# Kernel tuning notes

Measured on AMD Instinct MI355X. Metric: run time of the kernel, lower is better.

## Reference

```python
import jax, jax.numpy as jnp
import numpy as np

N_NODES = 100000
N_EDGES = 1600000
IN_F, HID, OUT_F, K = 64, 64, 16, 3


def gcn_conv(x, src, dst, deg_inv_sqrt, W, b):
    """One PyG-style GCNConv with precomputed self-loop-augmented edges & norm.
    x: [N, Fin]; src/dst: [E+N]; W: [Fin, Fout]; b: [Fout]."""
    h = x @ W                                  # [N, Fout]
    norm = deg_inv_sqrt[src] * deg_inv_sqrt[dst]  # [E+N]
    msg = h[src] * norm[:, None]               # gather + scale  [E+N, Fout]
    out = jax.ops.segment_sum(msg, dst, num_segments=x.shape[0])  # scatter-add
    return out + b


def _prep_edges(edge_index, n):
    loop = jnp.arange(n, dtype=edge_index.dtype)
    src = jnp.concatenate([edge_index[0], loop])
    dst = jnp.concatenate([edge_index[1], loop])
    deg = jax.ops.segment_sum(jnp.ones_like(dst, dtype=jnp.float32), dst, num_segments=n)
    deg_inv_sqrt = jnp.where(deg > 0, jax.lax.rsqrt(jnp.maximum(deg, 1.0)), 0.0)
    return src, dst, deg_inv_sqrt


def setup_inputs() -> dict:
    key = jax.random.key(0)
    ks = jax.random.split(key, 10)
    x = jax.random.normal(ks[0], (N_NODES, IN_F), dtype=jnp.float32)
    edge_index = jax.random.randint(ks[1], (2, N_EDGES), 0, N_NODES, dtype=jnp.int32)
    # Glorot-ish init for weights, zeros for biases (PyG default)
    def glorot(k, fin, fout):
        s = float(np.sqrt(6.0 / (fin + fout)))
        return jax.random.uniform(k, (fin, fout), jnp.float32, -s, s)
    W_in = glorot(ks[2], IN_F, HID)
    b_in = jnp.zeros((HID,), jnp.float32)
    W_h = jnp.stack([glorot(ks[3 + i], HID, HID) for i in range(K - 1)])  # [K-1, HID, HID]
    b_h = jnp.zeros((K - 1, HID), jnp.float32)
    W_out = glorot(ks[3 + K], HID, OUT_F)
    b_out = jnp.zeros((OUT_F,), jnp.float32)
    return {"x": x, "edge_index": edge_index, "W_in": W_in, "b_in": b_in,
            "W_h": W_h, "b_h": b_h, "W_out": W_out, "b_out": b_out}


def reference(x, edge_index, W_in, b_in, W_h, b_h, W_out, b_out):
    src, dst, dis = _prep_edges(edge_index, x.shape[0])
    h = jax.nn.relu(gcn_conv(x, src, dst, dis, W_in, b_in))
    for i in range(W_h.shape[0]):
        h = jax.nn.relu(gcn_conv(h, src, dst, dis, W_h[i], b_h[i]))
    return gcn_conv(h, src, dst, dis, W_out, b_out)
```

## Files before the change

### kernel.cpp

```cpp
#include <hip/hip_runtime.h>


#define BKT_SHIFT 7
#define BKT_NODES 128
#define NBMAX 800
#define EPT 16

typedef __attribute__((ext_vector_type(8))) short short8;
typedef __attribute__((ext_vector_type(4))) float f32x4;

union U4S8 { uint4 u; short8 s; };
__device__ __forceinline__ short8 as_s8(uint4 u) { U4S8 c; c.u = u; return c.s; }

__device__ __forceinline__ unsigned bf16rne(float f) {
    unsigned u = __float_as_uint(f);
    return (u + 0x7FFFu + ((u >> 16) & 1u)) >> 16;
}
__device__ __forceinline__ unsigned pack2(float a, float b) {
    return bf16rne(a) | (bf16rne(b) << 16);
}
__device__ __forceinline__ float lo16(unsigned u) { return __uint_as_float(u << 16); }
__device__ __forceinline__ float hi16(unsigned u) { return __uint_as_float(u & 0xFFFF0000u); }

__global__ __launch_bounds__(256) void k_bcount(const int* __restrict__ dst, int e,
                                                int* __restrict__ bcnt, int nb) {
    __shared__ int l[NBMAX];
    int tdx = threadIdx.x;
    for (int i = tdx; i < nb; i += 256) l[i] = 0;
    __syncthreads();
    int base = blockIdx.x * (256 * EPT);
#pragma unroll
    for (int k = 0; k < EPT; ++k) {
        int i = base + k * 256 + tdx;
        if (i < e) atomicAdd(&l[dst[i] >> BKT_SHIFT], 1);
    }
    __syncthreads();
    for (int i = tdx; i < nb; i += 256) {
        int c = l[i];
        if (c) atomicAdd(&bcnt[i], c);
    }
}

__global__ void k_bscan(const int* __restrict__ bcnt, int* __restrict__ bkt_off,
                        int* __restrict__ gcursor, int nb, int e) {
    __shared__ int lds[256];
    int tdx = threadIdx.x;
    int v[4], s = 0;
#pragma unroll
    for (int k = 0; k < 4; ++k) { int idx = tdx * 4 + k; v[k] = (idx < nb) ? bcnt[idx] : 0; s += v[k]; }
    lds[tdx] = s;
    __syncthreads();
    for (int off = 1; off < 256; off <<= 1) {
        int x = (tdx >= off) ? lds[tdx - off] : 0;
        __syncthreads();
        if (tdx >= off) lds[tdx] += x;
        __syncthreads();
    }
    int run = lds[tdx] - s;
#pragma unroll
    for (int k = 0; k < 4; ++k) {
        int idx = tdx * 4 + k;
        if (idx < nb) { bkt_off[idx] = run; gcursor[idx] = run; }
        run += v[k];
    }
    if (tdx == 0) bkt_off[nb] = e;
}

__global__ __launch_bounds__(256) void k_binB(const int* __restrict__ src,
                                              const int* __restrict__ dst, int e, int nb,
                                              int* __restrict__ gcursor,
                                              unsigned* __restrict__ bkt_edges) {
    __shared__ int lcnt[NBMAX];
    __shared__ int lbase[NBMAX];
    int tdx = threadIdx.x;
    for (int i = tdx; i < nb; i += 256) lcnt[i] = 0;
    __syncthreads();
    int base = blockIdx.x * (256 * EPT);
    unsigned val[EPT];
    int bkt[EPT];
#pragma unroll
    for (int k = 0; k < EPT; ++k) {
        int i = base + k * 256 + tdx;
        if (i < e) {
            int s_ = src[i], d_ = dst[i];
            val[k] = ((unsigned)s_ << BKT_SHIFT) | (unsigned)(d_ & (BKT_NODES - 1));
            bkt[k] = d_ >> BKT_SHIFT;
            atomicAdd(&lcnt[bkt[k]], 1);
        } else bkt[k] = -1;
    }
    __syncthreads();
    for (int b = tdx; b < nb; b += 256) {
        int c = lcnt[b];
        lbase[b] = c ? atomicAdd(&gcursor[b], c) : 0;
        lcnt[b] = 0;
    }
    __syncthreads();
#pragma unroll
    for (int k = 0; k < EPT; ++k) {
        if (bkt[k] >= 0) {
            int o = atomicAdd(&lcnt[bkt[k]], 1);
            bkt_edges[lbase[bkt[k]] + o] = val[k];
        }
    }
}

__global__ __launch_bounds__(256) void k_bsort(
    const int* __restrict__ bkt_off, const unsigned* __restrict__ bkt_edges,
    int* __restrict__ row_ptr, int* __restrict__ csr_src, float* __restrict__ dis,
    int n, int e, int nb) {
    __shared__ int hist[BKT_NODES];
    __shared__ int sc[BKT_NODES];
    __shared__ int cur[BKT_NODES];
    int b = blockIdx.x, tdx = threadIdx.x;
    int beg = bkt_off[b], end = bkt_off[b + 1];
    if (tdx < BKT_NODES) hist[tdx] = 0;
    __syncthreads();
    for (int j = beg + tdx; j < end; j += 256)
        atomicAdd(&hist[bkt_edges[j] & (BKT_NODES - 1)], 1);
    __syncthreads();
    if (tdx < BKT_NODES) sc[tdx] = hist[tdx];
    __syncthreads();
    for (int off = 1; off < BKT_NODES; off <<= 1) {
        int v = (tdx < BKT_NODES && tdx >= off) ? sc[tdx - off] : 0;
        __syncthreads();
        if (tdx < BKT_NODES && tdx >= off) sc[tdx] += v;
        __syncthreads();
    }
    if (tdx < BKT_NODES) {
        int node = b * BKT_NODES + tdx;
        if (node < n) {
            int pos = beg + sc[tdx] - hist[tdx];
            row_ptr[node] = pos;
            cur[tdx] = pos;
            dis[node] = rsqrtf((float)(hist[tdx] + 1));
        }
    }
    if (b == nb - 1 && tdx == 0) row_ptr[n] = e;
    __syncthreads();
    for (int j = beg + tdx; j < end; j += 256) {
        unsigned ev = bkt_edges[j];
        int p = atomicAdd(&cur[ev & (BKT_NODES - 1)], 1);
        csr_src[p] = (int)(ev >> BKT_SHIFT);
    }
}

__global__ void k_cvtX(const float4* __restrict__ x, uint2* __restrict__ hb, int n16) {
    int i = blockIdx.x * 256 + threadIdx.x;
    if (i < n16) {
        float4 v = x[i];
        hb[i] = make_uint2(pack2(v.x, v.y), pack2(v.z, v.w));
    }
}

__global__ void k_cvtW(const float* __restrict__ W, unsigned short* __restrict__ Wt) {
    int i = blockIdx.x * 256 + threadIdx.x;
    int col = i >> 6, k = i & 63;
    Wt[i] = (unsigned short)bf16rne(W[(size_t)k * 64 + col]);
}

__global__ __launch_bounds__(256) void k_mmfma(
    const uint4* __restrict__ hb,
    const uint4* __restrict__ Wt,
    const float* __restrict__ dis,
    unsigned short* __restrict__ t,
    int n) {
    int wave = threadIdx.x >> 6;
    int lane = threadIdx.x & 63;
    int base = blockIdx.x * 64 + wave * 16;
    if (base >= n) return;
    int l15 = lane & 15, lq = lane >> 4;

    int arow = base + l15;
    int arowc = arow < n ? arow : n - 1;
    short8 a0 = as_s8(hb[(size_t)arowc * 8 + lq]);
    short8 a1 = as_s8(hb[(size_t)arowc * 8 + 4 + lq]);

    int orow0 = base + lq * 4;
    float dn[4];
#pragma unroll
    for (int r = 0; r < 4; ++r) {
        int rr = orow0 + r;
        dn[r] = (rr < n) ? dis[rr] : 0.f;
    }

#pragma unroll
    for (int c = 0; c < 4; ++c) {
        short8 b0 = as_s8(Wt[(size_t)(c * 16 + l15) * 8 + lq]);
        short8 b1 = as_s8(Wt[(size_t)(c * 16 + l15) * 8 + 4 + lq]);
        f32x4 acc = {0.f, 0.f, 0.f, 0.f};
        acc = __builtin_amdgcn_mfma_f32_16x16x32_bf16(a0, b0, acc, 0, 0, 0);
        acc = __builtin_amdgcn_mfma_f32_16x16x32_bf16(a1, b1, acc, 0, 0, 0);
#pragma unroll
        for (int r = 0; r < 4; ++r) {
            int row = orow0 + r;
            if (row < n)
                t[(size_t)row * 64 + c * 16 + l15] = (unsigned short)bf16rne(acc[r] * dn[r]);
        }
    }
}

__global__ __launch_bounds__(256) void k_matmul16(
    const uint4* __restrict__ hb, const float* __restrict__ W,
    const float* __restrict__ dis, unsigned* __restrict__ tb, int n) {
    int row = blockIdx.x * 256 + threadIdx.x;
    if (row >= n) return;
    const float4* __restrict__ W4 = (const float4*)W;
    float4 acc[4];
#pragma unroll
    for (int j = 0; j < 4; ++j) acc[j] = make_float4(0.f, 0.f, 0.f, 0.f);
    for (int kq = 0; kq < 8; ++kq) {
        uint4 hv = hb[(size_t)row * 8 + kq];
        float xs[8];
        xs[0] = lo16(hv.x); xs[1] = hi16(hv.x); xs[2] = lo16(hv.y); xs[3] = hi16(hv.y);
        xs[4] = lo16(hv.z); xs[5] = hi16(hv.z); xs[6] = lo16(hv.w); xs[7] = hi16(hv.w);
#pragma unroll
        for (int j = 0; j < 8; ++j) {
            const float4* wr = W4 + (size_t)(kq * 8 + j) * 4;
            float4 w0 = wr[0], w1 = wr[1], w2 = wr[2], w3 = wr[3];
            acc[0].x = fmaf(xs[j], w0.x, acc[0].x); acc[0].y = fmaf(xs[j], w0.y, acc[0].y);
            acc[0].z = fmaf(xs[j], w0.z, acc[0].z); acc[0].w = fmaf(xs[j], w0.w, acc[0].w);
            acc[1].x = fmaf(xs[j], w1.x, acc[1].x); acc[1].y = fmaf(xs[j], w1.y, acc[1].y);
            acc[1].z = fmaf(xs[j], w1.z, acc[1].z); acc[1].w = fmaf(xs[j], w1.w, acc[1].w);
            acc[2].x = fmaf(xs[j], w2.x, acc[2].x); acc[2].y = fmaf(xs[j], w2.y, acc[2].y);
            acc[2].z = fmaf(xs[j], w2.z, acc[2].z); acc[2].w = fmaf(xs[j], w2.w, acc[2].w);
            acc[3].x = fmaf(xs[j], w3.x, acc[3].x); acc[3].y = fmaf(xs[j], w3.y, acc[3].y);
            acc[3].z = fmaf(xs[j], w3.z, acc[3].z); acc[3].w = fmaf(xs[j], w3.w, acc[3].w);
        }
    }
    float dn = dis[row];
    uint4* __restrict__ tr = (uint4*)(tb + (size_t)row * 8);
    uint4 o0;
    o0.x = pack2(acc[0].x * dn, acc[0].y * dn);
    o0.y = pack2(acc[0].z * dn, acc[0].w * dn);
    o0.z = pack2(acc[1].x * dn, acc[1].y * dn);
    o0.w = pack2(acc[1].z * dn, acc[1].w * dn);
    uint4 o1;
    o1.x = pack2(acc[2].x * dn, acc[2].y * dn);
    o1.y = pack2(acc[2].z * dn, acc[2].w * dn);
    o1.z = pack2(acc[3].x * dn, acc[3].y * dn);
    o1.w = pack2(acc[3].z * dn, acc[3].w * dn);
    tr[0] = o0;
    tr[1] = o1;
}

__global__ void k_gather64(const int* __restrict__ row_ptr, const int* __restrict__ csr_src,
                           const uint2* __restrict__ t2, const float* __restrict__ dis,
                           const float* __restrict__ b, uint2* __restrict__ hb2, int n) {
    int tid  = blockIdx.x * blockDim.x + threadIdx.x;
    int node = tid >> 4;
    if (node >= n) return;
    int lane15  = threadIdx.x & 15;
    int grpbase = threadIdx.x & 48;
    int beg = row_ptr[node], end = row_ptr[node + 1];

    uint2 sv0 = t2[(size_t)node * 16 + lane15];
    float4 acc = make_float4(lo16(sv0.x), hi16(sv0.x), lo16(sv0.y), hi16(sv0.y));

    for (int j0 = beg; j0 < end; j0 += 16) {
        int myj = j0 + lane15;
        int sv  = (myj < end) ? csr_src[myj] : 0;
        int m   = end - j0; if (m > 16) m = 16;
        int k = 0;
        for (; k + 4 <= m; k += 4) {
            int s0 = __shfl(sv, grpbase + k);
            int s1 = __shfl(sv, grpbase + k + 1);
            int s2 = __shfl(sv, grpbase + k + 2);
            int s3 = __shfl(sv, grpbase + k + 3);
            uint2 v0 = t2[(size_t)s0 * 16 + lane15];
            uint2 v1 = t2[(size_t)s1 * 16 + lane15];
            uint2 v2 = t2[(size_t)s2 * 16 + lane15];
            uint2 v3 = t2[(size_t)s3 * 16 + lane15];
            acc.x += lo16(v0.x); acc.y += hi16(v0.x); acc.z += lo16(v0.y); acc.w += hi16(v0.y);
            acc.x += lo16(v1.x); acc.y += hi16(v1.x); acc.z += lo16(v1.y); acc.w += hi16(v1.y);
            acc.x += lo16(v2.x); acc.y += hi16(v2.x); acc.z += lo16(v2.y); acc.w += hi16(v2.y);
            acc.x += lo16(v3.x); acc.y += hi16(v3.x); acc.z += lo16(v3.y); acc.w += hi16(v3.y);
        }
        for (; k < m; ++k) {
            int s0 = __shfl(sv, grpbase + k);
            uint2 v0 = t2[(size_t)s0 * 16 + lane15];
            acc.x += lo16(v0.x); acc.y += hi16(v0.x); acc.z += lo16(v0.y); acc.w += hi16(v0.y);
        }
    }
    float dn = dis[node];
    const float4 bb = *(const float4*)(b + lane15 * 4);
    float ox = fmaxf(fmaf(dn, acc.x, bb.x), 0.f);
    float oy = fmaxf(fmaf(dn, acc.y, bb.y), 0.f);
    float oz = fmaxf(fmaf(dn, acc.z, bb.z), 0.f);
    float ow = fmaxf(fmaf(dn, acc.w, bb.w), 0.f);
    hb2[(size_t)node * 16 + lane15] = make_uint2(pack2(ox, oy), pack2(oz, ow));
}

__global__ void k_gather16(const int* __restrict__ row_ptr, const int* __restrict__ csr_src,
                           const uint2* __restrict__ t2, const float* __restrict__ dis,
                           const float* __restrict__ b, float* __restrict__ out, int n) {
    int tid  = blockIdx.x * blockDim.x + threadIdx.x;
    int node = tid >> 2;
    if (node >= n) return;
    int lane3   = threadIdx.x & 3;
    int grpbase = threadIdx.x & 60;
    int beg = row_ptr[node], end = row_ptr[node + 1];

    uint2 sv0 = t2[(size_t)node * 4 + lane3];
    float4 acc = make_float4(lo16(sv0.x), hi16(sv0.x), lo16(sv0.y), hi16(sv0.y));

    for (int j0 = beg; j0 < end; j0 += 4) {
        int myj = j0 + lane3;
        int sv  = (myj < end) ? csr_src[myj] : 0;
        int m   = end - j0; if (m > 4) m = 4;
        int k = 0;
        for (; k + 2 <= m; k += 2) {
            int s0 = __shfl(sv, grpbase + k);
            int s1 = __shfl(sv, grpbase + k + 1);
            uint2 v0 = t2[(size_t)s0 * 4 + lane3];
            uint2 v1 = t2[(size_t)s1 * 4 + lane3];
            acc.x += lo16(v0.x); acc.y += hi16(v0.x); acc.z += lo16(v0.y); acc.w += hi16(v0.y);
            acc.x += lo16(v1.x); acc.y += hi16(v1.x); acc.z += lo16(v1.y); acc.w += hi16(v1.y);
        }
        for (; k < m; ++k) {
            int s0 = __shfl(sv, grpbase + k);
            uint2 v0 = t2[(size_t)s0 * 4 + lane3];
            acc.x += lo16(v0.x); acc.y += hi16(v0.x); acc.z += lo16(v0.y); acc.w += hi16(v0.y);
        }
    }
    float dn = dis[node];
    const float4 bb = *(const float4*)(b + lane3 * 4);
    float4 o;
    o.x = fmaf(dn, acc.x, bb.x);
    o.y = fmaf(dn, acc.y, bb.y);
    o.z = fmaf(dn, acc.z, bb.z);
    o.w = fmaf(dn, acc.w, bb.w);
    *(float4*)(out + (size_t)node * 16 + lane3 * 4) = o;
}


extern "C" void kernel_launch(void* const* d_in, const int* in_sizes, int n_in,
                              void* d_out, int out_size, void* d_ws, size_t ws_size,
                              hipStream_t stream) {
    const float* x     = (const float*)d_in[0];
    const int*   ei    = (const int*)d_in[1];
    const float* W_in  = (const float*)d_in[2];
    const float* b_in  = (const float*)d_in[3];
    const float* W_h   = (const float*)d_in[4];
    const float* b_h   = (const float*)d_in[5];
    const float* W_out = (const float*)d_in[6];
    const float* b_out = (const float*)d_in[7];

    const int n = in_sizes[0] / 64;
    const int e = in_sizes[1] / 2;
    const int* src = ei;
    const int* dst = ei + e;
    const int nb = (n + BKT_NODES - 1) / BKT_NODES;
    if (nb > NBMAX) return;

    char* ws = (char*)d_ws;
    size_t off = 0;
    auto alloc = [&](size_t bytes) { void* p = ws + off; off += (bytes + 255) & ~(size_t)255; return p; };
    float*          dis       = (float*)alloc((size_t)n * 4);
    unsigned short* hb        = (unsigned short*)alloc((size_t)n * 64 * 2);
    unsigned short* t         = (unsigned short*)alloc((size_t)n * 64 * 2);
    unsigned short* Wt        = (unsigned short*)alloc(3 * 4096 * 2);
    int*            bcnt      = (int*)alloc((size_t)nb * 4);
    int*            bkt_off   = (int*)alloc(((size_t)nb + 1) * 4);
    int*            gcursor   = (int*)alloc((size_t)nb * 4);
    unsigned*       bkt_edges = (unsigned*)alloc((size_t)e * 4);
    int*            row_ptr   = (int*)alloc(((size_t)n + 1) * 4);
    int*            csr_src   = (int*)alloc((size_t)e * 4);

    const int nblk_e = (e + 256 * EPT - 1) / (256 * EPT);
    const int nblk_m = (n + 63) / 64;

    hipMemsetAsync(bcnt, 0, (size_t)nb * 4, stream);
    k_bcount<<<nblk_e, 256, 0, stream>>>(dst, e, bcnt, nb);
    k_bscan <<<1, 256, 0, stream>>>(bcnt, bkt_off, gcursor, nb, e);
    k_binB  <<<nblk_e, 256, 0, stream>>>(src, dst, e, nb, gcursor, bkt_edges);
    k_bsort <<<nb, 256, 0, stream>>>(bkt_off, bkt_edges, row_ptr, csr_src, dis, n, e, nb);

    k_cvtW<<<16, 256, 0, stream>>>(W_in, Wt);
    k_cvtW<<<16, 256, 0, stream>>>(W_h, Wt + 4096);
    k_cvtW<<<16, 256, 0, stream>>>(W_h + 4096, Wt + 2 * 4096);
    k_cvtX<<<(n * 16 + 255) / 256, 256, 0, stream>>>((const float4*)x, (uint2*)hb, n * 16);

    k_mmfma<<<nblk_m, 256, 0, stream>>>((const uint4*)hb, (const uint4*)Wt, dis, t, n);
    k_gather64<<<(n * 16 + 255) / 256, 256, 0, stream>>>(row_ptr, csr_src, (const uint2*)t,
                                                         dis, b_in, (uint2*)hb, n);

    for (int l = 0; l < 2; ++l) {
        k_mmfma<<<nblk_m, 256, 0, stream>>>((const uint4*)hb, (const uint4*)(Wt + (1 + l) * 4096),
                                            dis, t, n);
        k_gather64<<<(n * 16 + 255) / 256, 256, 0, stream>>>(row_ptr, csr_src, (const uint2*)t,
                                                             dis, b_h + (size_t)l * 64,
                                                             (uint2*)hb, n);
    }

    k_matmul16<<<(n + 255) / 256, 256, 0, stream>>>((const uint4*)hb, W_out, dis, (unsigned*)t, n);
    k_gather16<<<(n * 4 + 255) / 256, 256, 0, stream>>>(row_ptr, csr_src, (const uint2*)t,
                                                        dis, b_out, (float*)d_out, n);
}
```

Baseline: 249.6 us.

## Fuse gather aggregation with next layer's MFMA matmul via LDS tile

After: 208.6 us. 16.4% less time.

```diff
diff --git a/kernel.cpp b/kernel.cpp
--- a/kernel.cpp
+++ b/kernel.cpp
@@ -144,36 +144,42 @@
     }
 }
 
-__global__ void k_cvtX(const float4* __restrict__ x, uint2* __restrict__ hb, int n16) {
+__global__ void k_cvtW(const float* __restrict__ W_in, const float* __restrict__ W_h,
+                       const float* __restrict__ W_out, unsigned short* __restrict__ Wt) {
     int i = blockIdx.x * 256 + threadIdx.x;
-    if (i < n16) {
-        float4 v = x[i];
-        hb[i] = make_uint2(pack2(v.x, v.y), pack2(v.z, v.w));
-    }
-}
-
-__global__ void k_cvtW(const float* __restrict__ W, unsigned short* __restrict__ Wt) {
-    int i = blockIdx.x * 256 + threadIdx.x;
-    int col = i >> 6, k = i & 63;
-    Wt[i] = (unsigned short)bf16rne(W[(size_t)k * 64 + col]);
-}
-
-__global__ __launch_bounds__(256) void k_mmfma(
-    const uint4* __restrict__ hb,
+    if (i < 12288) {
+        int w = i >> 12, r = i & 4095;
+        int col = r >> 6, k = r & 63;
+        const float* Wp = (w == 0) ? W_in : W_h + (size_t)(w - 1) * 4096;
+        Wt[i] = (unsigned short)bf16rne(Wp[(size_t)k * 64 + col]);
+    } else if (i < 13312) {
+        int r = i - 12288;
+        int col = r >> 6, k = r & 63;
+        Wt[i] = (unsigned short)bf16rne(W_out[(size_t)k * 16 + col]);
+    }
+}
+
+__global__ __launch_bounds__(256) void k_mmfma_x(
+    const float4* __restrict__ x4,
     const uint4* __restrict__ Wt,
     const float* __restrict__ dis,
-    unsigned short* __restrict__ t,
-    int n) {
-    int wave = threadIdx.x >> 6;
-    int lane = threadIdx.x & 63;
+    unsigned short* __restrict__ t, int n) {
+    int wave = threadIdx.x >> 6, lane = threadIdx.x & 63;
     int base = blockIdx.x * 64 + wave * 16;
     if (base >= n) return;
     int l15 = lane & 15, lq = lane >> 4;
 
     int arow = base + l15;
-    int arowc = arow < n ? arow : n - 1;
-    short8 a0 = as_s8(hb[(size_t)arowc * 8 + lq]);
-    short8 a1 = as_s8(hb[(size_t)arowc * 8 + 4 + lq]);
+    int ac = arow < n ? arow : n - 1;
+    const float4* xr = x4 + (size_t)ac * 16;
+    float4 f0 = xr[lq * 2], f1 = xr[lq * 2 + 1];
+    float4 f2 = xr[8 + lq * 2], f3 = xr[9 + lq * 2];
+    uint4 u0, u1;
+    u0.x = pack2(f0.x, f0.y); u0.y = pack2(f0.z, f0.w);
+    u0.z = pack2(f1.x, f1.y); u0.w = pack2(f1.z, f1.w);
+    u1.x = pack2(f2.x, f2.y); u1.y = pack2(f2.z, f2.w);
+    u1.z = pack2(f3.x, f3.y); u1.w = pack2(f3.z, f3.w);
+    short8 a0 = as_s8(u0), a1 = as_s8(u1);
 
     int orow0 = base + lq * 4;
     float dn[4];
@@ -182,7 +188,6 @@
         int rr = orow0 + r;
         dn[r] = (rr < n) ? dis[rr] : 0.f;
     }
-
 #pragma unroll
     for (int c = 0; c < 4; ++c) {
         short8 b0 = as_s8(Wt[(size_t)(c * 16 + l15) * 8 + lq]);
@@ -199,95 +204,95 @@
     }
 }
 
-__global__ __launch_bounds__(256) void k_matmul16(
-    const uint4* __restrict__ hb, const float* __restrict__ W,
-    const float* __restrict__ dis, unsigned* __restrict__ tb, int n) {
-    int row = blockIdx.x * 256 + threadIdx.x;
-    if (row >= n) return;
-    const float4* __restrict__ W4 = (const float4*)W;
-    float4 acc[4];
-#pragma unroll
-    for (int j = 0; j < 4; ++j) acc[j] = make_float4(0.f, 0.f, 0.f, 0.f);
-    for (int kq = 0; kq < 8; ++kq) {
-        uint4 hv = hb[(size_t)row * 8 + kq];
-        float xs[8];
-        xs[0] = lo16(hv.x); xs[1] = hi16(hv.x); xs[2] = lo16(hv.y); xs[3] = hi16(hv.y);
-        xs[4] = lo16(hv.z); xs[5] = hi16(hv.z); xs[6] = lo16(hv.w); xs[7] = hi16(hv.w);
-#pragma unroll
-        for (int j = 0; j < 8; ++j) {
-            const float4* wr = W4 + (size_t)(kq * 8 + j) * 4;
-            float4 w0 = wr[0], w1 = wr[1], w2 = wr[2], w3 = wr[3];
-            acc[0].x = fmaf(xs[j], w0.x, acc[0].x); acc[0].y = fmaf(xs[j], w0.y, acc[0].y);
-            acc[0].z = fmaf(xs[j], w0.z, acc[0].z); acc[0].w = fmaf(xs[j], w0.w, acc[0].w);
-            acc[1].x = fmaf(xs[j], w1.x, acc[1].x); acc[1].y = fmaf(xs[j], w1.y, acc[1].y);
-            acc[1].z = fmaf(xs[j], w1.z, acc[1].z); acc[1].w = fmaf(xs[j], w1.w, acc[1].w);
-            acc[2].x = fmaf(xs[j], w2.x, acc[2].x); acc[2].y = fmaf(xs[j], w2.y, acc[2].y);
-            acc[2].z = fmaf(xs[j], w2.z, acc[2].z); acc[2].w = fmaf(xs[j], w2.w, acc[2].w);
-            acc[3].x = fmaf(xs[j], w3.x, acc[3].x); acc[3].y = fmaf(xs[j], w3.y, acc[3].y);
-            acc[3].z = fmaf(xs[j], w3.z, acc[3].z); acc[3].w = fmaf(xs[j], w3.w, acc[3].w);
-        }
-    }
-    float dn = dis[row];
-    uint4* __restrict__ tr = (uint4*)(tb + (size_t)row * 8);
-    uint4 o0;
-    o0.x = pack2(acc[0].x * dn, acc[0].y * dn);
-    o0.y = pack2(acc[0].z * dn, acc[0].w * dn);
-    o0.z = pack2(acc[1].x * dn, acc[1].y * dn);
-    o0.w = pack2(acc[1].z * dn, acc[1].w * dn);
-    uint4 o1;
-    o1.x = pack2(acc[2].x * dn, acc[2].y * dn);
-    o1.y = pack2(acc[2].z * dn, acc[2].w * dn);
-    o1.z = pack2(acc[3].x * dn, acc[3].y * dn);
-    o1.w = pack2(acc[3].z * dn, acc[3].w * dn);
-    tr[0] = o0;
-    tr[1] = o1;
-}
-
-__global__ void k_gather64(const int* __restrict__ row_ptr, const int* __restrict__ csr_src,
-                           const uint2* __restrict__ t2, const float* __restrict__ dis,
-                           const float* __restrict__ b, uint2* __restrict__ hb2, int n) {
-    int tid  = blockIdx.x * blockDim.x + threadIdx.x;
-    int node = tid >> 4;
-    if (node >= n) return;
-    int lane15  = threadIdx.x & 15;
-    int grpbase = threadIdx.x & 48;
-    int beg = row_ptr[node], end = row_ptr[node + 1];
-
-    uint2 sv0 = t2[(size_t)node * 16 + lane15];
-    float4 acc = make_float4(lo16(sv0.x), hi16(sv0.x), lo16(sv0.y), hi16(sv0.y));
-
-    for (int j0 = beg; j0 < end; j0 += 16) {
-        int myj = j0 + lane15;
-        int sv  = (myj < end) ? csr_src[myj] : 0;
-        int m   = end - j0; if (m > 16) m = 16;
-        int k = 0;
-        for (; k + 4 <= m; k += 4) {
-            int s0 = __shfl(sv, grpbase + k);
-            int s1 = __shfl(sv, grpbase + k + 1);
-            int s2 = __shfl(sv, grpbase + k + 2);
-            int s3 = __shfl(sv, grpbase + k + 3);
-            uint2 v0 = t2[(size_t)s0 * 16 + lane15];
-            uint2 v1 = t2[(size_t)s1 * 16 + lane15];
-            uint2 v2 = t2[(size_t)s2 * 16 + lane15];
-            uint2 v3 = t2[(size_t)s3 * 16 + lane15];
-            acc.x += lo16(v0.x); acc.y += hi16(v0.x); acc.z += lo16(v0.y); acc.w += hi16(v0.y);
-            acc.x += lo16(v1.x); acc.y += hi16(v1.x); acc.z += lo16(v1.y); acc.w += hi16(v1.y);
-            acc.x += lo16(v2.x); acc.y += hi16(v2.x); acc.z += lo16(v2.y); acc.w += hi16(v2.y);
-            acc.x += lo16(v3.x); acc.y += hi16(v3.x); acc.z += lo16(v3.y); acc.w += hi16(v3.y);
-        }
-        for (; k < m; ++k) {
-            int s0 = __shfl(sv, grpbase + k);
-            uint2 v0 = t2[(size_t)s0 * 16 + lane15];
-            acc.x += lo16(v0.x); acc.y += hi16(v0.x); acc.z += lo16(v0.y); acc.w += hi16(v0.y);
-        }
-    }
-    float dn = dis[node];
-    const float4 bb = *(const float4*)(b + lane15 * 4);
-    float ox = fmaxf(fmaf(dn, acc.x, bb.x), 0.f);
-    float oy = fmaxf(fmaf(dn, acc.y, bb.y), 0.f);
-    float oz = fmaxf(fmaf(dn, acc.z, bb.z), 0.f);
-    float ow = fmaxf(fmaf(dn, acc.w, bb.w), 0.f);
-    hb2[(size_t)node * 16 + lane15] = make_uint2(pack2(ox, oy), pack2(oz, ow));
+template<int NC>
+__global__ __launch_bounds__(256) void k_fused(
+    const int* __restrict__ row_ptr, const int* __restrict__ csr_src,
+    const uint2* __restrict__ t_in,
+    const float* __restrict__ dis, const float* __restrict__ bias,
+    const uint4* __restrict__ Wt,
+    unsigned short* __restrict__ t_out, int n) {
+    __shared__ unsigned short htile[64][72];
+
+    int tdx = threadIdx.x;
+    int grp = tdx >> 4, l15 = tdx & 15;
+    int grpbase = tdx & 48;
+    int nblk0 = blockIdx.x * 64;
+
+    const float4 bb = *(const float4*)(bias + l15 * 4);
+
+#pragma unroll
+    for (int rnd = 0; rnd < 4; ++rnd) {
+        int nl = rnd * 16 + grp;
+        int node = nblk0 + nl;
+        uint2 hw = make_uint2(0u, 0u);
+        if (node < n) {
+            int beg = row_ptr[node], end = row_ptr[node + 1];
+            uint2 sv0 = t_in[(size_t)node * 16 + l15];
+            float4 acc = make_float4(lo16(sv0.x), hi16(sv0.x), lo16(sv0.y), hi16(sv0.y));
+            for (int j0 = beg; j0 < end; j0 += 16) {
+                int myj = j0 + l15;
+                int sv  = (myj < end) ? csr_src[myj] : 0;
+                int m   = end - j0; if (m > 16) m = 16;
+                int k = 0;
+                for (; k + 4 <= m; k += 4) {
+                    int s0 = __shfl(sv, grpbase + k);
+                    int s1 = __shfl(sv, grpbase + k + 1);
+                    int s2 = __shfl(sv, grpbase + k + 2);
+                    int s3 = __shfl(sv, grpbase + k + 3);
+                    uint2 v0 = t_in[(size_t)s0 * 16 + l15];
+                    uint2 v1 = t_in[(size_t)s1 * 16 + l15];
+                    uint2 v2 = t_in[(size_t)s2 * 16 + l15];
+                    uint2 v3 = t_in[(size_t)s3 * 16 + l15];
+                    acc.x += lo16(v0.x); acc.y += hi16(v0.x); acc.z += lo16(v0.y); acc.w += hi16(v0.y);
+                    acc.x += lo16(v1.x); acc.y += hi16(v1.x); acc.z += lo16(v1.y); acc.w += hi16(v1.y);
+                    acc.x += lo16(v2.x); acc.y += hi16(v2.x); acc.z += lo16(v2.y); acc.w += hi16(v2.y);
+                    acc.x += lo16(v3.x); acc.y += hi16(v3.x); acc.z += lo16(v3.y); acc.w += hi16(v3.y);
+                }
+                for (; k < m; ++k) {
+                    int s0 = __shfl(sv, grpbase + k);
+                    uint2 v0 = t_in[(size_t)s0 * 16 + l15];
+                    acc.x += lo16(v0.x); acc.y += hi16(v0.x); acc.z += lo16(v0.y); acc.w += hi16(v0.y);
+                }
+            }
+            float dn = dis[node];
+            float ox = fmaxf(fmaf(dn, acc.x, bb.x), 0.f);
+            float oy = fmaxf(fmaf(dn, acc.y, bb.y), 0.f);
+            float oz = fmaxf(fmaf(dn, acc.z, bb.z), 0.f);
+            float ow = fmaxf(fmaf(dn, acc.w, bb.w), 0.f);
+            hw = make_uint2(pack2(ox, oy), pack2(oz, ow));
+        }
+        *(uint2*)&htile[nl][l15 * 4] = hw;
+    }
+    __syncthreads();
+
+    int wave = tdx >> 6, lane = tdx & 63;
+    int lq = lane >> 4;
+    int rbase = wave * 16;
+    short8 a0 = as_s8(*(const uint4*)&htile[rbase + l15][lq * 8]);
+    short8 a1 = as_s8(*(const uint4*)&htile[rbase + l15][32 + lq * 8]);
+
+    int orow0 = nblk0 + rbase + lq * 4;
+    float dn[4];
+#pragma unroll
+    for (int r = 0; r < 4; ++r) {
+        int rr = orow0 + r;
+        dn[r] = (rr < n) ? dis[rr] : 0.f;
+    }
+#pragma unroll
+    for (int c = 0; c < NC; ++c) {
+        short8 b0 = as_s8(Wt[(size_t)(c * 16 + l15) * 8 + lq]);
+        short8 b1 = as_s8(Wt[(size_t)(c * 16 + l15) * 8 + 4 + lq]);
+        f32x4 acc = {0.f, 0.f, 0.f, 0.f};
+        acc = __builtin_amdgcn_mfma_f32_16x16x32_bf16(a0, b0, acc, 0, 0, 0);
+        acc = __builtin_amdgcn_mfma_f32_16x16x32_bf16(a1, b1, acc, 0, 0, 0);
+#pragma unroll
+        for (int r = 0; r < 4; ++r) {
+            int row = orow0 + r;
+            if (row < n)
+                t_out[(size_t)row * (NC * 16) + c * 16 + l15] =
+                    (unsigned short)bf16rne(acc[r] * dn[r]);
+        }
+    }
 }
 
 __global__ void k_gather16(const int* __restrict__ row_ptr, const int* __restrict__ csr_src,
@@ -356,9 +361,9 @@
     size_t off = 0;
     auto alloc = [&](size_t bytes) { void* p = ws + off; off += (bytes + 255) & ~(size_t)255; return p; };
     float*          dis       = (float*)alloc((size_t)n * 4);
-    unsigned short* hb        = (unsigned short*)alloc((size_t)n * 64 * 2);
-    unsigned short* t         = (unsigned short*)alloc((size_t)n * 64 * 2);
-    unsigned short* Wt        = (unsigned short*)alloc(3 * 4096 * 2);
+    unsigned short* t_a       = (unsigned short*)alloc((size_t)n * 64 * 2);
+    unsigned short* t_b       = (unsigned short*)alloc((size_t)n * 64 * 2);
+    unsigned short* Wt        = (unsigned short*)alloc(13312 * 2);
     int*            bcnt      = (int*)alloc((size_t)nb * 4);
     int*            bkt_off   = (int*)alloc(((size_t)nb + 1) * 4);
     int*            gcursor   = (int*)alloc((size_t)nb * 4);
@@ -367,7 +372,7 @@
     int*            csr_src   = (int*)alloc((size_t)e * 4);
 
     const int nblk_e = (e + 256 * EPT - 1) / (256 * EPT);
-    const int nblk_m = (n + 63) / 64;
+    const int nblk_f = (n + 63) / 64;
 
     hipMemsetAsync(bcnt, 0, (size_t)nb * 4, stream);
     k_bcount<<<nblk_e, 256, 0, stream>>>(dst, e, bcnt, nb);
@@ -375,24 +380,16 @@
     k_binB  <<<nblk_e, 256, 0, stream>>>(src, dst, e, nb, gcursor, bkt_edges);
     k_bsort <<<nb, 256, 0, stream>>>(bkt_off, bkt_edges, row_ptr, csr_src, dis, n, e, nb);
 
-    k_cvtW<<<16, 256, 0, stream>>>(W_in, Wt);
-    k_cvtW<<<16, 256, 0, stream>>>(W_h, Wt + 4096);
-    k_cvtW<<<16, 256, 0, stream>>>(W_h + 4096, Wt + 2 * 4096);
-    k_cvtX<<<(n * 16 + 255) / 256, 256, 0, stream>>>((const float4*)x, (uint2*)hb, n * 16);
-
-    k_mmfma<<<nblk_m, 256, 0, stream>>>((const uint4*)hb, (const uint4*)Wt, dis, t, n);
-    k_gather64<<<(n * 16 + 255) / 256, 256, 0, stream>>>(row_ptr, csr_src, (const uint2*)t,
-                                                         dis, b_in, (uint2*)hb, n);
-
-    for (int l = 0; l < 2; ++l) {
-        k_mmfma<<<nblk_m, 256, 0, stream>>>((const uint4*)hb, (const uint4*)(Wt + (1 + l) * 4096),
-                                            dis, t, n);
-        k_gather64<<<(n * 16 + 255) / 256, 256, 0, stream>>>(row_ptr, csr_src, (const uint2*)t,
-                                                             dis, b_h + (size_t)l * 64,
-                                                             (uint2*)hb, n);
-    }
-
-    k_matmul16<<<(n + 255) / 256, 256, 0, stream>>>((const uint4*)hb, W_out, dis, (unsigned*)t, n);
-    k_gather16<<<(n * 4 + 255) / 256, 256, 0, stream>>>(row_ptr, csr_src, (const uint2*)t,
+    k_cvtW<<<52, 256, 0, stream>>>(W_in, W_h, W_out, Wt);
+
+    k_mmfma_x<<<nblk_f, 256, 0, stream>>>((const float4*)x, (const uint4*)Wt, dis, t_a, n);
+
+    k_fused<4><<<nblk_f, 256, 0, stream>>>(row_ptr, csr_src, (const uint2*)t_a, dis, b_in,
+                                           (const uint4*)(Wt + 4096), t_b, n);
+    k_fused<4><<<nblk_f, 256, 0, stream>>>(row_ptr, csr_src, (const uint2*)t_b, dis, b_h,
+                                           (const uint4*)(Wt + 8192), t_a, n);
+    k_fused<1><<<nblk_f, 256, 0, stream>>>(row_ptr, csr_src, (const uint2*)t_a, dis, b_h + 64,
+                                           (const uint4*)(Wt + 12288), t_b, n);
+    k_gather16<<<(n * 4 + 255) / 256, 256, 0, stream>>>(row_ptr, csr_src, (const uint2*)t_b,
                                                         dis, b_out, (float*)d_out, n);
 }
```
